# Optimization experiments

Hardware: AMD Instinct MI355X
Metric: run time of the kernel (lower is better)

Reference implementation:

```python
import jax, jax.numpy as jnp
import numpy as np

B, L, D, H, NL = 4, 2048, 1024, 4, 2
HD = D // H
FF = 4 * D
EPS = 1e-5


def layernorm(x, g, b):
    mu = jnp.mean(x, axis=-1, keepdims=True)
    var = jnp.mean(jnp.square(x - mu), axis=-1, keepdims=True)
    return (x - mu) * jax.lax.rsqrt(var + EPS) * g + b


def setup_inputs() -> dict:
    key = jax.random.key(0)
    ks = jax.random.split(key, 8)
    std = 0.02
    return {
        "x": jax.random.normal(ks[0], (B, L, 3 * D), dtype=jnp.float32),
        "w3d": jax.random.normal(ks[1], (D, 3 * D), dtype=jnp.float32) * std,
        "b3d": jnp.zeros((D,), jnp.float32),
        "ln1_g": jnp.ones((NL, D), jnp.float32),
        "ln1_b": jnp.zeros((NL, D), jnp.float32),
        "wqkv": jax.random.normal(ks[2], (NL, 3 * D, D), dtype=jnp.float32) * std,
        "bqkv": jnp.zeros((NL, 3 * D), jnp.float32),
        "wproj": jax.random.normal(ks[3], (NL, D, D), dtype=jnp.float32) * std,
        "bproj": jnp.zeros((NL, D), jnp.float32),
        "ln2_g": jnp.ones((NL, D), jnp.float32),
        "ln2_b": jnp.zeros((NL, D), jnp.float32),
        "w1": jax.random.normal(ks[4], (NL, FF, D), dtype=jnp.float32) * std,
        "b1": jnp.zeros((NL, FF), jnp.float32),
        "w2": jax.random.normal(ks[5], (NL, D, FF), dtype=jnp.float32) * std,
        "b2": jnp.zeros((NL, D), jnp.float32),
        "lnf_g": jnp.ones((D,), jnp.float32),
        "lnf_b": jnp.zeros((D,), jnp.float32),
    }


def reference(x, w3d, b3d, ln1_g, ln1_b, wqkv, bqkv, wproj, bproj,
              ln2_g, ln2_b, w1, b1, w2, b2, lnf_g, lnf_b):
    h = jnp.einsum('bli,di->bld', x, w3d) + b3d
    scale = 1.0 / jnp.sqrt(jnp.float32(HD))
    for i in range(NL):
        # attention block
        res = h
        hn = layernorm(h, ln1_g[i], ln1_b[i])
        qkv = jnp.einsum('bld,ed->ble', hn, wqkv[i]) + bqkv[i]  # [B,L,3D]
        qkv = qkv.reshape(B, L, 3, H, HD)
        q, k, v = qkv[:, :, 0], qkv[:, :, 1], qkv[:, :, 2]  # [B,L,H,HD]
        attn = jnp.einsum('bqhd,bkhd->bhqk', q, k) * scale
        attn = jax.nn.softmax(attn, axis=-1)
        o = jnp.einsum('bhqk,bkhd->bqhd', attn, v).reshape(B, L, D)
        h = res + jnp.einsum('bld,ed->ble', o, wproj[i]) + bproj[i]
        # FFN block
        res = h
        hn = layernorm(h, ln2_g[i], ln2_b[i])
        f = jnp.einsum('bld,fd->blf', hn, w1[i]) + b1[i]
        f = jax.nn.gelu(f, approximate=False)  # torch nn.GELU default is exact
        h = res + jnp.einsum('blf,df->bld', f, w2[i]) + b2[i]
    return layernorm(h, lnf_g, lnf_b)
```

## Files before the change

kernel.cpp:

```cpp
#include <hip/hip_runtime.h>
#include <cstdint>
#include <cstddef>

#define BATCH   4
#define L_SEQ   2048
#define DMODEL  1024
#define NHEAD   4
#define HDIM    256
#define FFDIM   4096
#define MROWS   (BATCH * L_SEQ)
#define NLAYER  2

typedef __bf16 bf16_t;
typedef __bf16 bf16x8 __attribute__((ext_vector_type(8)));
typedef __bf16 bf16x4 __attribute__((ext_vector_type(4)));
typedef float  floatx4 __attribute__((ext_vector_type(4)));

__device__ __forceinline__ void async_cp16(const void* g, void* l) {
  auto gp = reinterpret_cast<__attribute__((address_space(1))) void*>(
      reinterpret_cast<uintptr_t>(g));
  auto lp = reinterpret_cast<__attribute__((address_space(3))) void*>(
      reinterpret_cast<uintptr_t>(l));
  __builtin_amdgcn_global_load_lds(gp, lp, 16, 0, 0);
}

__global__ __launch_bounds__(256)
void cvt_f32_bf16(const float* __restrict__ in, bf16_t* __restrict__ out, int n4) {
  int i = blockIdx.x * 256 + threadIdx.x;
  if (i >= n4) return;
  float4 v = ((const float4*)in)[i];
  bf16x4 ov = { (bf16_t)v.x, (bf16_t)v.y, (bf16_t)v.z, (bf16_t)v.w };
  ((bf16x4*)out)[i] = ov;
}

template<bool BF16OUT>
__global__ __launch_bounds__(256)
void ln_kernel(const float* __restrict__ x, const float* __restrict__ gw,
               const float* __restrict__ bw, void* __restrict__ outp) {
  const int row = blockIdx.x;
  const int tid = threadIdx.x;
  const float4 v = ((const float4*)(x + (size_t)row * DMODEL))[tid];
  float s  = v.x + v.y + v.z + v.w;
  float ss = v.x * v.x + v.y * v.y + v.z * v.z + v.w * v.w;
#pragma unroll
  for (int o = 32; o > 0; o >>= 1) {
    s  += __shfl_xor(s, o);
    ss += __shfl_xor(ss, o);
  }
  __shared__ float red0[4], red1[4];
  const int wv = tid >> 6;
  if ((tid & 63) == 0) { red0[wv] = s; red1[wv] = ss; }
  __syncthreads();
  s  = red0[0] + red0[1] + red0[2] + red0[3];
  ss = red1[0] + red1[1] + red1[2] + red1[3];
  const float mu  = s * (1.0f / DMODEL);
  const float var = ss * (1.0f / DMODEL) - mu * mu;
  const float rs  = rsqrtf(var + 1e-5f);
  const float4 g4 = ((const float4*)gw)[tid];
  const float4 b4 = ((const float4*)bw)[tid];
  const float o0 = (v.x - mu) * rs * g4.x + b4.x;
  const float o1 = (v.y - mu) * rs * g4.y + b4.y;
  const float o2 = (v.z - mu) * rs * g4.z + b4.z;
  const float o3 = (v.w - mu) * rs * g4.w + b4.w;
  if (BF16OUT) {
    bf16x4 ov = { (bf16_t)o0, (bf16_t)o1, (bf16_t)o2, (bf16_t)o3 };
    ((bf16x4*)outp)[(size_t)row * (DMODEL / 4) + tid] = ov;
  } else {
    float4 ov = { o0, o1, o2, o3 };
    ((float4*)outp)[(size_t)row * (DMODEL / 4) + tid] = ov;
  }
}

__global__ __launch_bounds__(512, 2)
void flash_attn(const bf16_t* __restrict__ Q, const bf16_t* __restrict__ K,
                const bf16_t* __restrict__ VT, bf16_t* __restrict__ O) {
  __shared__ bf16_t lsK[64 * 256];
  __shared__ bf16_t lsV[256 * 64];
  const int tid = threadIdx.x, wave = tid >> 6, lane = tid & 63;
  const int lane15 = lane & 15, quad = lane >> 4;
  const int z = blockIdx.y, qt = blockIdx.x;
  const bf16_t* Qz = Q + (size_t)z * L_SEQ * HDIM;
  const bf16_t* Kz = K + (size_t)z * L_SEQ * HDIM;
  const bf16_t* Vz = VT + (size_t)z * HDIM * L_SEQ;

  const int qrow = qt * 128 + wave * 16 + lane15;
  bf16x8 qf[8];
#pragma unroll
  for (int kc = 0; kc < 8; ++kc)
    qf[kc] = *(const bf16x8*)(Qz + (size_t)qrow * HDIM + kc * 32 + quad * 8);

  floatx4 oacc[16] = {};
  float m_run = -1e30f, l_run = 0.f;

  const int krl = lane >> 5, kp = lane & 31;
  const int vrl = lane >> 3, vp = lane & 7;
  bf16_t* Pw = lsK + wave * 1024;

  for (int kt = 0; kt < L_SEQ; kt += 64) {
#pragma unroll
    for (int j = 0; j < 4; ++j) {
      const int i = wave * 4 + j;
      const int r = 2 * i + krl;
      const int col = ((kp & 24) | ((kp ^ r) & 7)) * 8;
      async_cp16(Kz + (size_t)(kt + r) * HDIM + col, lsK + i * 512);
      const int rv = 8 * i + vrl;
      const int colv = ((vp ^ rv) & 7) * 8;
      async_cp16(Vz + (size_t)rv * L_SEQ + kt + colv, lsV + i * 512);
    }
    __syncthreads();

    floatx4 sacc[4] = {};
#pragma unroll
    for (int kc = 0; kc < 8; ++kc) {
#pragma unroll
      for (int mf = 0; mf < 4; ++mf) {
        const int rr = mf * 16 + lane15;
        const int c = kc * 4 + quad;
        const int phys = (c & 24) | ((c ^ rr) & 7);
        bf16x8 af = *(const bf16x8*)(lsK + rr * 256 + phys * 8);
        sacc[mf] = __builtin_amdgcn_mfma_f32_16x16x32_bf16(af, qf[kc],
                                                           sacc[mf], 0, 0, 0);
      }
    }

    float p[4][4];
    float mx = -1e30f;
#pragma unroll
    for (int mf = 0; mf < 4; ++mf)
#pragma unroll
      for (int r = 0; r < 4; ++r) {
        p[mf][r] = sacc[mf][r] * 0.0625f;
        mx = fmaxf(mx, p[mf][r]);
      }
    mx = fmaxf(mx, __shfl_xor(mx, 16));
    mx = fmaxf(mx, __shfl_xor(mx, 32));
    const float m_new = fmaxf(m_run, mx);
    const float alpha = __expf(m_run - m_new);
    float rs = 0.f;
#pragma unroll
    for (int mf = 0; mf < 4; ++mf)
#pragma unroll
      for (int r = 0; r < 4; ++r) {
        p[mf][r] = __expf(p[mf][r] - m_new);
        rs += p[mf][r];
      }
    rs += __shfl_xor(rs, 16);
    rs += __shfl_xor(rs, 32);
    l_run = l_run * alpha + rs;
    m_run = m_new;
#pragma unroll
    for (int mf = 0; mf < 16; ++mf)
#pragma unroll
      for (int r = 0; r < 4; ++r) oacc[mf][r] *= alpha;

    __syncthreads();

#pragma unroll
    for (int mf = 0; mf < 4; ++mf) {
      bf16x4 pk = { (bf16_t)p[mf][0], (bf16_t)p[mf][1],
                    (bf16_t)p[mf][2], (bf16_t)p[mf][3] };
      const int c = mf * 2 + (quad >> 1);
      const int phys = c ^ (lane15 & 7);
      *(bf16x4*)(Pw + lane15 * 64 + phys * 8 + (quad & 1) * 4) = pk;
    }

#pragma unroll
    for (int kc = 0; kc < 2; ++kc) {
      const int cb = kc * 4 + quad;
      const int pb = cb ^ (lane15 & 7);
      bf16x8 bfr = *(const bf16x8*)(Pw + lane15 * 64 + pb * 8);
#pragma unroll
      for (int mf = 0; mf < 16; ++mf) {
        const int rr = mf * 16 + lane15;
        const int phys = cb ^ (rr & 7);
        bf16x8 af = *(const bf16x8*)(lsV + rr * 64 + phys * 8);
        oacc[mf] = __builtin_amdgcn_mfma_f32_16x16x32_bf16(af, bfr,
                                                           oacc[mf], 0, 0, 0);
      }
    }
    __syncthreads();
  }

  const float inv = 1.0f / l_run;
  const int b = z >> 2, head = z & 3;
  bf16_t* orow = O + ((size_t)b * L_SEQ + qrow) * DMODEL + head * HDIM;
#pragma unroll
  for (int mf = 0; mf < 16; ++mf) {
    const int hd = mf * 16 + quad * 4;
    bf16x4 ov = { (bf16_t)(oacc[mf][0] * inv), (bf16_t)(oacc[mf][1] * inv),
                  (bf16_t)(oacc[mf][2] * inv), (bf16_t)(oacc[mf][3] * inv) };
    *(bf16x4*)(orow + hd) = ov;
  }
}

struct EpiBiasF32 {
  float* C; const float* bias; int ldc;
  __device__ __forceinline__ void store4(int, int m, int n, floatx4 v) const {
    const float bb = bias[n];
#pragma unroll
    for (int r = 0; r < 4; ++r) C[(size_t)(m + r) * ldc + n] = v[r] + bb;
  }
};
struct EpiResBiasF32 {
  float* C; const float* bias; int ldc;
  __device__ __forceinline__ void store4(int, int m, int n, floatx4 v) const {
    const float bb = bias[n];
#pragma unroll
    for (int r = 0; r < 4; ++r) {
      const size_t idx = (size_t)(m + r) * ldc + n;
      C[idx] = C[idx] + v[r] + bb;
    }
  }
};
struct EpiGeluBf16 {
  bf16_t* C; const float* bias; int ldc;
  __device__ __forceinline__ void store4(int, int m, int n, floatx4 v) const {
    const float bb = bias[n];
#pragma unroll
    for (int r = 0; r < 4; ++r) {
      const float t = v[r] + bb;
      const float g = 0.5f * t * (1.0f + erff(t * 0.7071067811865475f));
      C[(size_t)(m + r) * ldc + n] = (bf16_t)g;
    }
  }
};
struct EpiQKV {
  bf16_t *q, *k, *vT; const float* bias;
  __device__ __forceinline__ void store4(int, int m, int n, floatx4 v) const {
    const float bb = bias[n];
    const int b = m >> 11, l = m & 2047;
    const int which = n >> 10, e = n & 1023;
    const int head = e >> 8, hd = e & 255;
    const int z = b * NHEAD + head;
    if (which == 2) {
      bf16x4 ov = { (bf16_t)(v[0] + bb), (bf16_t)(v[1] + bb),
                    (bf16_t)(v[2] + bb), (bf16_t)(v[3] + bb) };
      *(bf16x4*)(vT + ((size_t)z * HDIM + hd) * L_SEQ + l) = ov;
    } else {
      bf16_t* dst = (which == 0 ? q : k) + ((size_t)z * L_SEQ + l) * HDIM + hd;
#pragma unroll
      for (int r = 0; r < 4; ++r) dst[(size_t)r * HDIM] = (bf16_t)(v[r] + bb);
    }
  }
};

template<class Epi>
__global__ __launch_bounds__(256, 3)
void gemm_bt(const bf16_t* __restrict__ A, int lda, long strideA,
             const bf16_t* __restrict__ B, int ldb, long strideB,
             int K, Epi epi) {
  __shared__ bf16_t lsA[128 * 64];
  __shared__ bf16_t lsB[128 * 64];
  const int tid  = threadIdx.x;
  const int wave = tid >> 6, lane = tid & 63;
  const int z = blockIdx.z;
  A += (size_t)z * strideA;
  B += (size_t)z * strideB;
  const int m0 = blockIdx.y * 128, n0 = blockIdx.x * 128;

  const int rl = lane >> 3, p = lane & 7;
  const int csw = (p ^ rl) * 8;
  const int rbase = wave * 32 + rl;
  const bf16_t* gA = A + (size_t)(m0 + rbase) * lda + csw;
  const bf16_t* gB = B + (size_t)(n0 + rbase) * ldb + csw;
  bf16_t* lA = &lsA[wave * 32 * 64];
  bf16_t* lB = &lsB[wave * 32 * 64];

  const int wm = wave >> 1, wn = wave & 1;
  const int lane15 = lane & 15, quad = lane >> 4;
  const int arow = wm * 64 + lane15;
  const int brow = wn * 64 + lane15;
  const int sw = lane15 & 7;
  const int koff0 = ((quad + 0) ^ sw) * 8;
  const int koff1 = ((quad + 4) ^ sw) * 8;

  floatx4 acc[4][4] = {};

  for (int k0 = 0; k0 < K; k0 += 64) {
#pragma unroll
    for (int j = 0; j < 4; ++j) {
      async_cp16(gA + k0 + (size_t)j * 8 * lda, lA + j * 8 * 64);
      async_cp16(gB + k0 + (size_t)j * 8 * ldb, lB + j * 8 * 64);
    }
    __syncthreads();
#pragma unroll
    for (int kk = 0; kk < 2; ++kk) {
      const int ko = kk ? koff1 : koff0;
      bf16x8 af[4], bfr[4];
#pragma unroll
      for (int i = 0; i < 4; ++i)
        af[i] = *(const bf16x8*)&lsA[(arow + i * 16) * 64 + ko];
#pragma unroll
      for (int j = 0; j < 4; ++j)
        bfr[j] = *(const bf16x8*)&lsB[(brow + j * 16) * 64 + ko];
#pragma unroll
      for (int i = 0; i < 4; ++i)
#pragma unroll
        for (int j = 0; j < 4; ++j)
          acc[i][j] = __builtin_amdgcn_mfma_f32_16x16x32_bf16(af[i], bfr[j],
                                                              acc[i][j], 0, 0, 0);
    }
    __syncthreads();
  }

#pragma unroll
  for (int i = 0; i < 4; ++i) {
    const int mbase = m0 + wm * 64 + i * 16 + quad * 4;
#pragma unroll
    for (int j = 0; j < 4; ++j) {
      const int nloc = n0 + wn * 64 + j * 16 + lane15;
      epi.store4(z, mbase, nloc, acc[i][j]);
    }
  }
}

extern "C" void kernel_launch(void* const* d_in, const int* in_sizes, int n_in,
                              void* d_out, int out_size, void* d_ws, size_t ws_size,
                              hipStream_t stream) {
  const float* x_in  = (const float*)d_in[0];
  const float* w3d   = (const float*)d_in[1];
  const float* b3d   = (const float*)d_in[2];
  const float* ln1g  = (const float*)d_in[3];
  const float* ln1b  = (const float*)d_in[4];
  const float* wqkv  = (const float*)d_in[5];
  const float* bqkv  = (const float*)d_in[6];
  const float* wproj = (const float*)d_in[7];
  const float* bproj = (const float*)d_in[8];
  const float* ln2g  = (const float*)d_in[9];
  const float* ln2b  = (const float*)d_in[10];
  const float* w1    = (const float*)d_in[11];
  const float* b1    = (const float*)d_in[12];
  const float* w2    = (const float*)d_in[13];
  const float* b2    = (const float*)d_in[14];
  const float* lnfg  = (const float*)d_in[15];
  const float* lnfb  = (const float*)d_in[16];
  float* out = (float*)d_out;

  char* ws = (char*)d_ws;
  size_t off = 0;
  auto alloc = [&](size_t bytes) -> void* {
    void* p = ws + off;
    off = (off + bytes + 255) & ~(size_t)255;
    return p;
  };
  float*  h      = (float*) alloc((size_t)MROWS * DMODEL * 4);
  bf16_t* hn     = (bf16_t*)alloc((size_t)MROWS * DMODEL * 2);
  bf16_t* w3db   = (bf16_t*)alloc((size_t)DMODEL * 3 * DMODEL * 2);
  bf16_t* wqkvb  = (bf16_t*)alloc((size_t)NLAYER * 3 * DMODEL * DMODEL * 2);
  bf16_t* wprojb = (bf16_t*)alloc((size_t)NLAYER * DMODEL * DMODEL * 2);
  bf16_t* w1b    = (bf16_t*)alloc((size_t)NLAYER * FFDIM * DMODEL * 2);
  bf16_t* w2b    = (bf16_t*)alloc((size_t)NLAYER * DMODEL * FFDIM * 2);
  bf16_t* xb     = (bf16_t*)alloc((size_t)MROWS * 3 * DMODEL * 2);
  bf16_t* qb     = (bf16_t*)alloc((size_t)MROWS * DMODEL * 2);
  bf16_t* kb     = (bf16_t*)alloc((size_t)MROWS * DMODEL * 2);
  bf16_t* vT     = (bf16_t*)alloc((size_t)MROWS * DMODEL * 2);
  bf16_t* ob     = (bf16_t*)alloc((size_t)MROWS * DMODEL * 2);
  bf16_t* f      = (bf16_t*)alloc((size_t)MROWS * FFDIM * 2);
  (void)ws_size; (void)in_sizes; (void)n_in; (void)out_size;

  auto cvt = [&](const float* src, bf16_t* dst, size_t n) {
    int n4 = (int)(n / 4);
    cvt_f32_bf16<<<(n4 + 255) / 256, 256, 0, stream>>>(src, dst, n4);
  };
  cvt(x_in,  xb,     (size_t)MROWS * 3 * DMODEL);
  cvt(w3d,   w3db,   (size_t)DMODEL * 3 * DMODEL);
  cvt(wqkv,  wqkvb,  (size_t)NLAYER * 3 * DMODEL * DMODEL);
  cvt(wproj, wprojb, (size_t)NLAYER * DMODEL * DMODEL);
  cvt(w1,    w1b,    (size_t)NLAYER * FFDIM * DMODEL);
  cvt(w2,    w2b,    (size_t)NLAYER * DMODEL * FFDIM);

  gemm_bt<<<dim3(DMODEL / 128, MROWS / 128, 1), 256, 0, stream>>>(
      xb, 3 * DMODEL, 0L, w3db, 3 * DMODEL, 0L, 3 * DMODEL,
      EpiBiasF32{h, b3d, DMODEL});

  for (int i = 0; i < NLAYER; ++i) {
    ln_kernel<true><<<MROWS, 256, 0, stream>>>(h, ln1g + i * DMODEL,
                                               ln1b + i * DMODEL, hn);
    gemm_bt<<<dim3(3 * DMODEL / 128, MROWS / 128, 1), 256, 0, stream>>>(
        hn, DMODEL, 0L, wqkvb + (size_t)i * 3 * DMODEL * DMODEL, DMODEL, 0L,
        DMODEL, EpiQKV{qb, kb, vT, bqkv + i * 3 * DMODEL});
    flash_attn<<<dim3(L_SEQ / 128, BATCH * NHEAD), 512, 0, stream>>>(
        qb, kb, vT, ob);
    gemm_bt<<<dim3(DMODEL / 128, MROWS / 128, 1), 256, 0, stream>>>(
        ob, DMODEL, 0L, wprojb + (size_t)i * DMODEL * DMODEL, DMODEL, 0L,
        DMODEL, EpiResBiasF32{h, bproj + i * DMODEL, DMODEL});
    ln_kernel<true><<<MROWS, 256, 0, stream>>>(h, ln2g + i * DMODEL,
                                               ln2b + i * DMODEL, hn);
    gemm_bt<<<dim3(FFDIM / 128, MROWS / 128, 1), 256, 0, stream>>>(
        hn, DMODEL, 0L, w1b + (size_t)i * FFDIM * DMODEL, DMODEL, 0L, DMODEL,
        EpiGeluBf16{f, b1 + i * FFDIM, FFDIM});
    gemm_bt<<<dim3(DMODEL / 128, MROWS / 128, 1), 256, 0, stream>>>(
        f, FFDIM, 0L, w2b + (size_t)i * DMODEL * FFDIM, FFDIM, 0L, FFDIM,
        EpiResBiasF32{h, b2 + i * DMODEL, DMODEL});
  }

  ln_kernel<false><<<MROWS, 256, 0, stream>>>(h, lnfg, lnfb, out);
}
```

Before: 1.281 ms.

## Split attention over key halves with a combine pass, two query tiles per wave

Flash attention now splits the key sequence into two halves along a new grid dimension. Each block writes unnormalized fp32 partial outputs plus running max and sum, and a new combine kernel merges the two halves into bf16. Each wave now handles two 16-row query groups with 256 threads per block, so every K/V fragment loaded from LDS feeds two MFMAs. This doubles the grid for more parallelism and raises LDS reuse, at the cost of extra fp32 partial-output traffic (reusing the FFN buffer), a second launch, and higher register pressure from two accumulator sets.

```diff
diff --git a/kernel.cpp b/kernel.cpp
--- a/kernel.cpp
+++ b/kernel.cpp
@@ -71,35 +71,40 @@
   }
 }
 
-__global__ __launch_bounds__(512, 2)
+__global__ __launch_bounds__(256, 2)
 void flash_attn(const bf16_t* __restrict__ Q, const bf16_t* __restrict__ K,
-                const bf16_t* __restrict__ VT, bf16_t* __restrict__ O) {
+                const bf16_t* __restrict__ VT, float* __restrict__ Opart,
+                float* __restrict__ ml) {
   __shared__ bf16_t lsK[64 * 256];
   __shared__ bf16_t lsV[256 * 64];
   const int tid = threadIdx.x, wave = tid >> 6, lane = tid & 63;
   const int lane15 = lane & 15, quad = lane >> 4;
-  const int z = blockIdx.y, qt = blockIdx.x;
+  const int z = blockIdx.y, qt = blockIdx.x, h = blockIdx.z;
   const bf16_t* Qz = Q + (size_t)z * L_SEQ * HDIM;
-  const bf16_t* Kz = K + (size_t)z * L_SEQ * HDIM;
-  const bf16_t* Vz = VT + (size_t)z * HDIM * L_SEQ;
-
-  const int qrow = qt * 128 + wave * 16 + lane15;
-  bf16x8 qf[8];
-#pragma unroll
-  for (int kc = 0; kc < 8; ++kc)
-    qf[kc] = *(const bf16x8*)(Qz + (size_t)qrow * HDIM + kc * 32 + quad * 8);
-
-  floatx4 oacc[16] = {};
-  float m_run = -1e30f, l_run = 0.f;
+  const bf16_t* Kz = K + ((size_t)z * L_SEQ + h * 1024) * HDIM;
+  const bf16_t* Vz = VT + (size_t)z * HDIM * L_SEQ + h * 1024;
+  float* Op = Opart + (size_t)h * MROWS * DMODEL;
+
+  bf16x8 qf[2][8];
+#pragma unroll
+  for (int g = 0; g < 2; ++g) {
+    const int qrow = qt * 128 + wave * 32 + g * 16 + lane15;
+#pragma unroll
+    for (int kc = 0; kc < 8; ++kc)
+      qf[g][kc] =
+          *(const bf16x8*)(Qz + (size_t)qrow * HDIM + kc * 32 + quad * 8);
+  }
+
+  floatx4 oacc[2][16] = {};
+  float m_run[2] = {-1e30f, -1e30f}, l_run[2] = {0.f, 0.f};
 
   const int krl = lane >> 5, kp = lane & 31;
   const int vrl = lane >> 3, vp = lane & 7;
-  bf16_t* Pw = lsK + wave * 1024;
-
-  for (int kt = 0; kt < L_SEQ; kt += 64) {
-#pragma unroll
-    for (int j = 0; j < 4; ++j) {
-      const int i = wave * 4 + j;
+
+  for (int kt = 0; kt < 1024; kt += 64) {
+#pragma unroll
+    for (int j = 0; j < 8; ++j) {
+      const int i = wave * 8 + j;
       const int r = 2 * i + krl;
       const int col = ((kp & 24) | ((kp ^ r) & 7)) * 8;
       async_cp16(Kz + (size_t)(kt + r) * HDIM + col, lsK + i * 512);
@@ -109,7 +114,7 @@
     }
     __syncthreads();
 
-    floatx4 sacc[4] = {};
+    floatx4 sacc[2][4] = {};
 #pragma unroll
     for (int kc = 0; kc < 8; ++kc) {
 #pragma unroll
@@ -118,79 +123,126 @@
         const int c = kc * 4 + quad;
         const int phys = (c & 24) | ((c ^ rr) & 7);
         bf16x8 af = *(const bf16x8*)(lsK + rr * 256 + phys * 8);
-        sacc[mf] = __builtin_amdgcn_mfma_f32_16x16x32_bf16(af, qf[kc],
-                                                           sacc[mf], 0, 0, 0);
+        sacc[0][mf] = __builtin_amdgcn_mfma_f32_16x16x32_bf16(af, qf[0][kc],
+                                                              sacc[0][mf], 0, 0, 0);
+        sacc[1][mf] = __builtin_amdgcn_mfma_f32_16x16x32_bf16(af, qf[1][kc],
+                                                              sacc[1][mf], 0, 0, 0);
       }
     }
 
-    float p[4][4];
-    float mx = -1e30f;
-#pragma unroll
-    for (int mf = 0; mf < 4; ++mf)
-#pragma unroll
-      for (int r = 0; r < 4; ++r) {
-        p[mf][r] = sacc[mf][r] * 0.0625f;
-        mx = fmaxf(mx, p[mf][r]);
+    bf16x4 pk[2][4];
+#pragma unroll
+    for (int g = 0; g < 2; ++g) {
+      float p[4][4];
+      float mx = -1e30f;
+#pragma unroll
+      for (int mf = 0; mf < 4; ++mf)
+#pragma unroll
+        for (int r = 0; r < 4; ++r) {
+          p[mf][r] = sacc[g][mf][r] * 0.0625f;
+          mx = fmaxf(mx, p[mf][r]);
+        }
+      mx = fmaxf(mx, __shfl_xor(mx, 16));
+      mx = fmaxf(mx, __shfl_xor(mx, 32));
+      const float m_new = fmaxf(m_run[g], mx);
+      const float alpha = __expf(m_run[g] - m_new);
+      float rs = 0.f;
+#pragma unroll
+      for (int mf = 0; mf < 4; ++mf) {
+#pragma unroll
+        for (int r = 0; r < 4; ++r) {
+          p[mf][r] = __expf(p[mf][r] - m_new);
+          rs += p[mf][r];
+        }
+        pk[g][mf] = bf16x4{ (bf16_t)p[mf][0], (bf16_t)p[mf][1],
+                            (bf16_t)p[mf][2], (bf16_t)p[mf][3] };
       }
-    mx = fmaxf(mx, __shfl_xor(mx, 16));
-    mx = fmaxf(mx, __shfl_xor(mx, 32));
-    const float m_new = fmaxf(m_run, mx);
-    const float alpha = __expf(m_run - m_new);
-    float rs = 0.f;
-#pragma unroll
-    for (int mf = 0; mf < 4; ++mf)
-#pragma unroll
-      for (int r = 0; r < 4; ++r) {
-        p[mf][r] = __expf(p[mf][r] - m_new);
-        rs += p[mf][r];
+      rs += __shfl_xor(rs, 16);
+      rs += __shfl_xor(rs, 32);
+      l_run[g] = l_run[g] * alpha + rs;
+      m_run[g] = m_new;
+#pragma unroll
+      for (int mf = 0; mf < 16; ++mf)
+#pragma unroll
+        for (int r = 0; r < 4; ++r) oacc[g][mf][r] *= alpha;
+    }
+
+    __syncthreads();
+
+#pragma unroll
+    for (int g = 0; g < 2; ++g) {
+      bf16_t* Pw = lsK + (wave * 2 + g) * 1024;
+#pragma unroll
+      for (int mf = 0; mf < 4; ++mf) {
+        const int c = mf * 2 + (quad >> 1);
+        const int phys = c ^ (lane15 & 7);
+        *(bf16x4*)(Pw + lane15 * 64 + phys * 8 + (quad & 1) * 4) = pk[g][mf];
       }
-    rs += __shfl_xor(rs, 16);
-    rs += __shfl_xor(rs, 32);
-    l_run = l_run * alpha + rs;
-    m_run = m_new;
-#pragma unroll
-    for (int mf = 0; mf < 16; ++mf)
-#pragma unroll
-      for (int r = 0; r < 4; ++r) oacc[mf][r] *= alpha;
-
-    __syncthreads();
-
-#pragma unroll
-    for (int mf = 0; mf < 4; ++mf) {
-      bf16x4 pk = { (bf16_t)p[mf][0], (bf16_t)p[mf][1],
-                    (bf16_t)p[mf][2], (bf16_t)p[mf][3] };
-      const int c = mf * 2 + (quad >> 1);
-      const int phys = c ^ (lane15 & 7);
-      *(bf16x4*)(Pw + lane15 * 64 + phys * 8 + (quad & 1) * 4) = pk;
     }
 
 #pragma unroll
     for (int kc = 0; kc < 2; ++kc) {
       const int cb = kc * 4 + quad;
       const int pb = cb ^ (lane15 & 7);
-      bf16x8 bfr = *(const bf16x8*)(Pw + lane15 * 64 + pb * 8);
+      bf16x8 bfr0 = *(const bf16x8*)(lsK + (wave * 2 + 0) * 1024 +
+                                     lane15 * 64 + pb * 8);
+      bf16x8 bfr1 = *(const bf16x8*)(lsK + (wave * 2 + 1) * 1024 +
+                                     lane15 * 64 + pb * 8);
 #pragma unroll
       for (int mf = 0; mf < 16; ++mf) {
         const int rr = mf * 16 + lane15;
         const int phys = cb ^ (rr & 7);
         bf16x8 af = *(const bf16x8*)(lsV + rr * 64 + phys * 8);
-        oacc[mf] = __builtin_amdgcn_mfma_f32_16x16x32_bf16(af, bfr,
-                                                           oacc[mf], 0, 0, 0);
+        oacc[0][mf] = __builtin_amdgcn_mfma_f32_16x16x32_bf16(af, bfr0,
+                                                              oacc[0][mf], 0, 0, 0);
+        oacc[1][mf] = __builtin_amdgcn_mfma_f32_16x16x32_bf16(af, bfr1,
+                                                              oacc[1][mf], 0, 0, 0);
       }
     }
     __syncthreads();
   }
 
-  const float inv = 1.0f / l_run;
   const int b = z >> 2, head = z & 3;
-  bf16_t* orow = O + ((size_t)b * L_SEQ + qrow) * DMODEL + head * HDIM;
-#pragma unroll
-  for (int mf = 0; mf < 16; ++mf) {
-    const int hd = mf * 16 + quad * 4;
-    bf16x4 ov = { (bf16_t)(oacc[mf][0] * inv), (bf16_t)(oacc[mf][1] * inv),
-                  (bf16_t)(oacc[mf][2] * inv), (bf16_t)(oacc[mf][3] * inv) };
-    *(bf16x4*)(orow + hd) = ov;
-  }
+#pragma unroll
+  for (int g = 0; g < 2; ++g) {
+    const int qrow = qt * 128 + wave * 32 + g * 16 + lane15;
+    float* orow = Op + ((size_t)b * L_SEQ + qrow) * DMODEL + head * HDIM;
+#pragma unroll
+    for (int mf = 0; mf < 16; ++mf) {
+      const int hd = mf * 16 + quad * 4;
+      floatx4 ov = oacc[g][mf];
+      *(floatx4*)(orow + hd) = ov;
+    }
+    if (quad == 0) {
+      float* mlp = ml + ((size_t)(h * 16 + z) * L_SEQ + qrow) * 2;
+      mlp[0] = m_run[g];
+      mlp[1] = l_run[g];
+    }
+  }
+}
+
+__global__ __launch_bounds__(256)
+void combine_attn(const float* __restrict__ Opart, const float* __restrict__ ml,
+                  bf16_t* __restrict__ ob) {
+  const int idx4 = blockIdx.x * 256 + threadIdx.x;
+  const int row = idx4 >> 8;
+  const int d = (idx4 & 255) * 4;
+  const int head = d >> 8;
+  const int b = row >> 11, l = row & 2047;
+  const int z = b * NHEAD + head;
+  const float* ml1 = ml + ((size_t)z * L_SEQ + l) * 2;
+  const float* ml2 = ml + ((size_t)(16 + z) * L_SEQ + l) * 2;
+  const float m1 = ml1[0], l1 = ml1[1], m2 = ml2[0], l2 = ml2[1];
+  const float m = fmaxf(m1, m2);
+  const float a1 = __expf(m1 - m), a2 = __expf(m2 - m);
+  const float inv = 1.0f / (l1 * a1 + l2 * a2);
+  const float4 o1 = ((const float4*)Opart)[idx4];
+  const float4 o2 = ((const float4*)(Opart + (size_t)MROWS * DMODEL))[idx4];
+  bf16x4 ov = { (bf16_t)((o1.x * a1 + o2.x * a2) * inv),
+                (bf16_t)((o1.y * a1 + o2.y * a2) * inv),
+                (bf16_t)((o1.z * a1 + o2.z * a2) * inv),
+                (bf16_t)((o1.w * a1 + o2.w * a2) * inv) };
+  ((bf16x4*)ob)[idx4] = ov;
 }
 
 struct EpiBiasF32 {
@@ -356,6 +408,8 @@
   bf16_t* vT     = (bf16_t*)alloc((size_t)MROWS * DMODEL * 2);
   bf16_t* ob     = (bf16_t*)alloc((size_t)MROWS * DMODEL * 2);
   bf16_t* f      = (bf16_t*)alloc((size_t)MROWS * FFDIM * 2);
+  float*  ml     = (float*) alloc(2ull * 16 * L_SEQ * 2 * 4);
+  float*  Opart  = (float*)f;
   (void)ws_size; (void)in_sizes; (void)n_in; (void)out_size;
 
   auto cvt = [&](const float* src, bf16_t* dst, size_t n) {
@@ -379,8 +433,9 @@
     gemm_bt<<<dim3(3 * DMODEL / 128, MROWS / 128, 1), 256, 0, stream>>>(
         hn, DMODEL, 0L, wqkvb + (size_t)i * 3 * DMODEL * DMODEL, DMODEL, 0L,
         DMODEL, EpiQKV{qb, kb, vT, bqkv + i * 3 * DMODEL});
-    flash_attn<<<dim3(L_SEQ / 128, BATCH * NHEAD), 512, 0, stream>>>(
-        qb, kb, vT, ob);
+    flash_attn<<<dim3(L_SEQ / 128, BATCH * NHEAD, 2), 256, 0, stream>>>(
+        qb, kb, vT, Opart, ml);
+    combine_attn<<<(MROWS * DMODEL / 4) / 256, 256, 0, stream>>>(Opart, ml, ob);
     gemm_bt<<<dim3(DMODEL / 128, MROWS / 128, 1), 256, 0, stream>>>(
         ob, DMODEL, 0L, wprojb + (size_t)i * DMODEL * DMODEL, DMODEL, 0L,
         DMODEL, EpiResBiasF32{h, bproj + i * DMODEL, DMODEL});
```

Result: slower. 1.426 ms (+11.4%).
